# Kernel tuning notes

Measured on AMD Instinct MI355X. Metric: run time of the kernel, lower is better.

Reference implementation:

```python
import jax, jax.numpy as jnp
import numpy as np

EPSILON = 1e-5
CUT_LO, CUT_HI = 0.0, 5.0


def _exp_normal_smear(dist, num_rbf):
    # dist: (..., 1) broadcast against num_rbf means -> (..., num_rbf)
    start = float(np.exp(-CUT_HI + CUT_LO))
    means = jnp.linspace(start, 1.0, num_rbf, dtype=dist.dtype)
    betas = jnp.full((num_rbf,), (2.0 / num_rbf * (1.0 - start)) ** -2, dtype=dist.dtype)
    alpha = 5.0 / (CUT_HI - CUT_LO)
    cutoff = 0.5 * (jnp.cos(np.pi * dist / CUT_HI) + 1.0) * (dist < CUT_HI)
    return cutoff * jnp.exp(-betas * (jnp.exp(alpha * (-dist + CUT_LO)) - means) ** 2)


def setup_inputs() -> dict:
    key = jax.random.key(0)
    k1, k2, k3, _ = jax.random.split(key, 4)
    B, N, K, H, O = 4, 16, 16, 64, 1
    x = jax.random.normal(k1, (B, N, 3), dtype=jnp.float32) * 3.0  # atom coords
    W = jax.random.normal(k2, (N, N, N, N, K, H), dtype=jnp.float32) * 0.02
    w_fc = jax.random.normal(k3, (H, O), dtype=jnp.float32) * 0.1
    b_fc = jnp.zeros((O,), dtype=jnp.float32)
    return {"x": x, "W": W, "w_fc": w_fc, "b_fc": b_fc}


def reference(x, W, w_fc, b_fc):
    # x: (B, N, 3); W: (N, N, N, N, K, H)
    K = W.shape[-2]
    diff = x[..., :, None, :] - x[..., None, :, :]          # (B, N, N, 3)
    norm_sq = jnp.sum(diff * diff, axis=-1, keepdims=True) + EPSILON  # (B, N, N, 1)
    norm = jnp.sqrt(norm_sq)
    diff = diff / norm_sq                                     # note: divide by norm^2 (faithful)
    smear = _exp_normal_smear(norm, K)                        # (B, N, N, K)
    basis = smear[..., None] * diff[..., None, :]             # (B, N, N, K, 3)
    h = jnp.einsum('zabkc,zdekc,abdeko->zao', basis, basis, W)  # (B, N, H)
    return jax.nn.silu(h) @ w_fc + b_fc                       # (B, N, O)
```

## Files before the change

### kernel.cpp

```cpp
#include <hip/hip_runtime.h>
#include <math.h>


#define NJ 65536
#define BPA 128

typedef float f32x4 __attribute__((ext_vector_type(4)));

static constexpr double D_START = 0.006737946999085467;

__device__ __forceinline__ bool pair_basis(const float* __restrict__ x,
                                           int z, int p, int q, int k,
                                           float& bx, float& by, float& bz) {
    const float* xp = x + (z * 16 + p) * 3;
    const float* xq = x + (z * 16 + q) * 3;
    float d0 = xp[0] - xq[0], d1 = xp[1] - xq[1], d2 = xp[2] - xq[2];
    float nsq = d0 * d0 + d1 * d1 + d2 * d2 + 1e-5f;
    float nrm = sqrtf(nsq);
    if (nrm >= 5.0f) return false;
    float cut = 0.5f * (cosf(nrm * 0.6283185307179586f) + 1.0f);
    float ex = expf(-nrm);
    const float START = (float)D_START;
    const float STEP  = (float)((1.0 - D_START) / 15.0);
    const float BETA  = (float)(1.0 / ((0.125 * (1.0 - D_START)) * (0.125 * (1.0 - D_START))));
    float m = START + STEP * (float)k;
    float dmm = ex - m;
    float s = cut * expf(-BETA * dmm * dmm) / nsq;
    bx = s * d0; by = s * d1; bz = s * d2;
    return true;
}

__global__ __launch_bounds__(256) void k_main(const f32x4* __restrict__ W4,
                                              const float* __restrict__ x,
                                              float* __restrict__ part) {
    int a   = blockIdx.x >> 7;
    int blk = blockIdx.x & (BPA - 1);

    __shared__ f32x4 p_lds[512];
    __shared__ float red[4][256];

    int t = threadIdx.x;
    f32x4 p0 = {0.f, 0.f, 0.f, 0.f}, p1 = {0.f, 0.f, 0.f, 0.f};
    {
        int e = t >> 4, k = t & 15;
        int b = blk >> 3, dd = (blk & 7) * 2;
        #pragma unroll
        for (int z = 0; z < 4; ++z) {
            float ux, uy, uz;
            if (pair_basis(x, z, a, b, k, ux, uy, uz)) {
                float vx, vy, vz;
                if (pair_basis(x, z, dd, e, k, vx, vy, vz))
                    p0[z] = ux * vx + uy * vy + uz * vz;
                if (pair_basis(x, z, dd + 1, e, k, vx, vy, vz))
                    p1[z] = ux * vx + uy * vy + uz * vz;
            }
        }
    }
    bool f0 = (fabsf(p0.x) + fabsf(p0.y) + fabsf(p0.z) + fabsf(p0.w)) != 0.0f;
    bool f1 = (fabsf(p1.x) + fabsf(p1.y) + fabsf(p1.z) + fabsf(p1.w)) != 0.0f;
    unsigned long long bal0 = __ballot(f0);
    unsigned long long bal1 = __ballot(f1);
    p_lds[t]       = p0;
    p_lds[t + 256] = p1;
    __syncthreads();

    int wave = threadIdx.x >> 6;
    int lane = threadIdx.x & 63;
    int og   = lane & 15;
    int rsub = lane >> 4;

    unsigned mask = 0;
    #pragma unroll
    for (int g = 0; g < 8; ++g) {
        if ((bal0 >> (8 * g)) & 0xFFull) mask |= 1u << g;
        if ((bal1 >> (8 * g)) & 0xFFull) mask |= 1u << (g + 8);
    }

    float acc[4][4] = {{0.f, 0.f, 0.f, 0.f}, {0.f, 0.f, 0.f, 0.f},
                       {0.f, 0.f, 0.f, 0.f}, {0.f, 0.f, 0.f, 0.f}};
    size_t rowbase = (size_t)a * NJ + (size_t)blk * 512;
    while (mask) {
        int g = __builtin_ctz(mask);
        mask &= mask - 1;
        int rloc = ((g & 8) ? 256 : 0) + wave * 64 + (g & 7) * 8 + rsub;
        f32x4 pA = p_lds[rloc];
        f32x4 pB = p_lds[rloc + 4];
        f32x4 wA = W4[(rowbase + rloc) * 16 + og];
        f32x4 wB = W4[(rowbase + rloc + 4) * 16 + og];
        acc[0][0] += pA.x * wA.x + pB.x * wB.x; acc[0][1] += pA.x * wA.y + pB.x * wB.y;
        acc[0][2] += pA.x * wA.z + pB.x * wB.z; acc[0][3] += pA.x * wA.w + pB.x * wB.w;
        acc[1][0] += pA.y * wA.x + pB.y * wB.x; acc[1][1] += pA.y * wA.y + pB.y * wB.y;
        acc[1][2] += pA.y * wA.z + pB.y * wB.z; acc[1][3] += pA.y * wA.w + pB.y * wB.w;
        acc[2][0] += pA.z * wA.x + pB.z * wB.x; acc[2][1] += pA.z * wA.y + pB.z * wB.y;
        acc[2][2] += pA.z * wA.z + pB.z * wB.z; acc[2][3] += pA.z * wA.w + pB.z * wB.w;
        acc[3][0] += pA.w * wA.x + pB.w * wB.x; acc[3][1] += pA.w * wA.y + pB.w * wB.y;
        acc[3][2] += pA.w * wA.z + pB.w * wB.z; acc[3][3] += pA.w * wA.w + pB.w * wB.w;
    }
    #pragma unroll
    for (int z = 0; z < 4; ++z) {
        #pragma unroll
        for (int c = 0; c < 4; ++c) {
            float v = acc[z][c];
            v += __shfl_xor(v, 16);
            v += __shfl_xor(v, 32);
            acc[z][c] = v;
        }
    }
    if (rsub == 0) {
        #pragma unroll
        for (int z = 0; z < 4; ++z) {
            #pragma unroll
            for (int c = 0; c < 4; ++c)
                red[wave][z * 64 + og * 4 + c] = acc[z][c];
        }
    }
    __syncthreads();
    float s = red[0][t] + red[1][t] + red[2][t] + red[3][t];
    part[((size_t)a * BPA + blk) * 256 + t] = s;
}

__global__ void k_out(const float* __restrict__ part, const float* __restrict__ w_fc,
                      const float* __restrict__ b_fc, float* __restrict__ out) {
    int z = blockIdx.x >> 4, a = blockIdx.x & 15;
    int o = threadIdx.x & 63, bq = threadIdx.x >> 6;
    float s = 0.f;
    for (int blk = bq; blk < BPA; blk += 4)
        s += part[((size_t)a * BPA + blk) * 256 + z * 64 + o];
    __shared__ float red[4][64];
    red[bq][o] = s;
    __syncthreads();
    if (threadIdx.x < 64) {
        float h = red[0][o] + red[1][o] + red[2][o] + red[3][o];
        float v = h * (1.0f / (1.0f + expf(-h))) * w_fc[o];
        #pragma unroll
        for (int off = 32; off >= 1; off >>= 1) v += __shfl_xor(v, off);
        if (o == 0) out[z * 16 + a] = v + b_fc[0];
    }
}

extern "C" void kernel_launch(void* const* d_in, const int* in_sizes, int n_in,
                              void* d_out, int out_size, void* d_ws, size_t ws_size,
                              hipStream_t stream) {
    const float* x    = (const float*)d_in[0];
    const float* W    = (const float*)d_in[1];
    const float* w_fc = (const float*)d_in[2];
    const float* b_fc = (const float*)d_in[3];
    float* ws = (float*)d_ws;

    float* part = ws;
    float* out  = (float*)d_out;

    k_main<<<16 * BPA, 256, 0, stream>>>((const f32x4*)W, x, part);
    k_out<<<64, 256, 0, stream>>>(part, w_fc, b_fc, out);
}
```

Measured before the change: 29.34 us.

## Precompute pair basis table in separate kernel and scramble block order

Adds a small pre-kernel that computes the smeared basis vector for every (z,p,q,k) once and stores it in workspace. The main kernel loads these instead of recomputing up to twelve transcendental-heavy basis evaluations per thread. Block indices are also permuted with a multiplicative hash, which may spread W reads across memory channels. The cost is an extra kernel launch and a global round trip for the basis table.

```diff
diff --git a/kernel.cpp b/kernel.cpp
--- a/kernel.cpp
+++ b/kernel.cpp
@@ -9,51 +9,59 @@
 
 static constexpr double D_START = 0.006737946999085467;
 
-__device__ __forceinline__ bool pair_basis(const float* __restrict__ x,
-                                           int z, int p, int q, int k,
-                                           float& bx, float& by, float& bz) {
+__global__ void k_basis(const float* __restrict__ x, f32x4* __restrict__ basisv) {
+    int t = blockIdx.x * 256 + threadIdx.x;
+    if (t >= 1024) return;
+    int q = t & 15, p = (t >> 4) & 15, z = t >> 8;
     const float* xp = x + (z * 16 + p) * 3;
     const float* xq = x + (z * 16 + q) * 3;
     float d0 = xp[0] - xq[0], d1 = xp[1] - xq[1], d2 = xp[2] - xq[2];
     float nsq = d0 * d0 + d1 * d1 + d2 * d2 + 1e-5f;
     float nrm = sqrtf(nsq);
-    if (nrm >= 5.0f) return false;
+    f32x4* o = basisv + (size_t)t * 16;
+    if (nrm >= 5.0f) {
+        f32x4 zv = {0.f, 0.f, 0.f, 0.f};
+        #pragma unroll
+        for (int k = 0; k < 16; ++k) o[k] = zv;
+        return;
+    }
     float cut = 0.5f * (cosf(nrm * 0.6283185307179586f) + 1.0f);
     float ex = expf(-nrm);
     const float START = (float)D_START;
     const float STEP  = (float)((1.0 - D_START) / 15.0);
     const float BETA  = (float)(1.0 / ((0.125 * (1.0 - D_START)) * (0.125 * (1.0 - D_START))));
-    float m = START + STEP * (float)k;
-    float dmm = ex - m;
-    float s = cut * expf(-BETA * dmm * dmm) / nsq;
-    bx = s * d0; by = s * d1; bz = s * d2;
-    return true;
+    #pragma unroll
+    for (int k = 0; k < 16; ++k) {
+        float m = START + STEP * (float)k;
+        float dmm = ex - m;
+        float s = cut * expf(-BETA * dmm * dmm) / nsq;
+        f32x4 v; v.x = s * d0; v.y = s * d1; v.z = s * d2; v.w = 0.f;
+        o[k] = v;
+    }
 }
 
 __global__ __launch_bounds__(256) void k_main(const f32x4* __restrict__ W4,
-                                              const float* __restrict__ x,
+                                              const f32x4* __restrict__ basisv,
                                               float* __restrict__ part) {
-    int a   = blockIdx.x >> 7;
-    int blk = blockIdx.x & (BPA - 1);
+    unsigned item = (blockIdx.x * 1237u) & 2047u;
+    int a   = (int)(item >> 7);
+    int blk = (int)(item & (BPA - 1));
 
     __shared__ f32x4 p_lds[512];
     __shared__ float red[4][256];
 
     int t = threadIdx.x;
-    f32x4 p0 = {0.f, 0.f, 0.f, 0.f}, p1 = {0.f, 0.f, 0.f, 0.f};
+    f32x4 p0, p1;
     {
         int e = t >> 4, k = t & 15;
         int b = blk >> 3, dd = (blk & 7) * 2;
         #pragma unroll
         for (int z = 0; z < 4; ++z) {
-            float ux, uy, uz;
-            if (pair_basis(x, z, a, b, k, ux, uy, uz)) {
-                float vx, vy, vz;
-                if (pair_basis(x, z, dd, e, k, vx, vy, vz))
-                    p0[z] = ux * vx + uy * vy + uz * vz;
-                if (pair_basis(x, z, dd + 1, e, k, vx, vy, vz))
-                    p1[z] = ux * vx + uy * vy + uz * vz;
-            }
+            f32x4 u  = basisv[(z * 256 + a * 16 + b) * 16 + k];
+            f32x4 v0 = basisv[(z * 256 + dd * 16 + e) * 16 + k];
+            f32x4 v1 = basisv[(z * 256 + (dd + 1) * 16 + e) * 16 + k];
+            p0[z] = u.x * v0.x + u.y * v0.y + u.z * v0.z;
+            p1[z] = u.x * v1.x + u.y * v1.y + u.z * v1.z;
         }
     }
     bool f0 = (fabsf(p0.x) + fabsf(p0.y) + fabsf(p0.z) + fabsf(p0.w)) != 0.0f;
@@ -145,11 +153,13 @@
     const float* W    = (const float*)d_in[1];
     const float* w_fc = (const float*)d_in[2];
     const float* b_fc = (const float*)d_in[3];
-    float* ws = (float*)d_ws;
+    float* ws  = (float*)d_ws;
+    float* out = (float*)d_out;
 
-    float* part = ws;
-    float* out  = (float*)d_out;
+    float* part   = ws;
+    f32x4* basisv = (f32x4*)(ws + 524288);
 
-    k_main<<<16 * BPA, 256, 0, stream>>>((const f32x4*)W, x, part);
+    k_basis<<<4, 256, 0, stream>>>(x, basisv);
+    k_main<<<16 * BPA, 256, 0, stream>>>((const f32x4*)W, basisv, part);
     k_out<<<64, 256, 0, stream>>>(part, w_fc, b_fc, out);
 }
```

Result: slower. 31.10 us (+6.0%).
